# Performance work log

Measured on AMD Instinct MI355X. Metric: run time of the kernel, lower is better.

## Reference

```python
import jax, jax.numpy as jnp
import numpy as np

D_MODEL = 1024
NUM_HEADS = 16
D_K = D_MODEL // NUM_HEADS  # 64
B, T = 2, 2048


def rope_tables(seq_len, d_k):
    # Matches RotaryPositionalEmbedding + the slice apply_rotary takes:
    # only cos/sin of freqs (dim d_k//2) are used.
    half = d_k // 2
    inv_freq = 1.0 / (10000.0 ** (jnp.arange(0, d_k, 2, dtype=jnp.float32) / d_k))  # (half,)
    t = jnp.arange(seq_len, dtype=jnp.float32)
    freqs = jnp.einsum('i,j->ij', t, inv_freq)  # (T, half)
    return jnp.cos(freqs), jnp.sin(freqs)


def apply_rotary(x, cos, sin):
    # x: (B, H, T, D); rotate first 2*half dims as two halves
    half = x.shape[-1] // 2
    x1, x2 = x[..., :half], x[..., half:2 * half]
    c = cos[None, None, :x.shape[2], :half]
    s = sin[None, None, :x.shape[2], :half]
    return jnp.concatenate([x1 * c - x2 * s, x1 * s + x2 * c], axis=-1)


def setup_inputs() -> dict:
    key = jax.random.key(0)
    ks = jax.random.split(key, 5)
    scale = 1.0 / np.sqrt(D_MODEL)
    return {
        'x': jax.random.normal(ks[0], (B, T, D_MODEL), dtype=jnp.float32),
        'wq': jax.random.normal(ks[1], (D_MODEL, D_MODEL), dtype=jnp.float32) * scale,
        'wk': jax.random.normal(ks[2], (D_MODEL, D_MODEL), dtype=jnp.float32) * scale,
        'wv': jax.random.normal(ks[3], (D_MODEL, D_MODEL), dtype=jnp.float32) * scale,
        'wo': jax.random.normal(ks[4], (D_MODEL, D_MODEL), dtype=jnp.float32) * scale,
    }


def reference(x, wq, wk, wv, wo):
    Bs, Ts, _ = x.shape
    def proj(w):
        # nn.Linear: x @ w.T, then split heads -> (B, H, T, d_k)
        return (x @ w.T).reshape(Bs, Ts, NUM_HEADS, D_K).transpose(0, 2, 1, 3)
    Q, K, V = proj(wq), proj(wk), proj(wv)
    cos, sin = rope_tables(Ts, D_K)
    Q = apply_rotary(Q, cos, sin)
    K = apply_rotary(K, cos, sin)
    scores = jnp.einsum('bhqd,bhkd->bhqk', Q, K) / jnp.sqrt(jnp.float32(D_K))
    attn = jax.nn.softmax(scores, axis=-1)  # dropout is identity in eval
    out = jnp.einsum('bhqk,bhkd->bhqd', attn, V)
    out = out.transpose(0, 2, 1, 3).reshape(Bs, Ts, D_MODEL)
    return out @ wo.T
```

## Files before the change

### kernel.cpp

```cpp
#include <hip/hip_runtime.h>
#include <math.h>

typedef __attribute__((ext_vector_type(8))) short short8;
typedef __attribute__((ext_vector_type(4))) short short4v;
typedef __attribute__((ext_vector_type(4))) float f32x4;
typedef __attribute__((ext_vector_type(16))) float f32x16;

#define D_MODEL 1024
#define NUM_HEADS 16
#define D_K 64
#define B_SZ 2
#define T_SZ 2048
#define M_ROWS (B_SZ * T_SZ)
#define LSTR 72
#define LOG2E 1.4426950408889634f
#define KVSPLIT 1024

__device__ __forceinline__ unsigned short f2bf(float f) {
    union { float f; unsigned int u; } v; v.f = f;
    unsigned int r = v.u + 0x7FFF + ((v.u >> 16) & 1);
    return (unsigned short)(r >> 16);
}
__device__ __forceinline__ void gload_lds16(const void* g, void* l) {
    __builtin_amdgcn_global_load_lds(
        (const __attribute__((address_space(1))) unsigned int*)g,
        (__attribute__((address_space(3))) unsigned int*)l, 16, 0, 0);
}
__device__ __forceinline__ int cvtpk(float lo, float hi) {
    int r;
    asm("v_cvt_pk_bf16_f32 %0, %1, %2" : "=v"(r) : "v"(lo), "v"(hi));
    return r;
}

__global__ __launch_bounds__(256) void cvt_all(
    const float* __restrict__ x,  const float* __restrict__ w0,
    const float* __restrict__ w1, const float* __restrict__ w2,
    const float* __restrict__ w3, unsigned short* __restrict__ dst)
{
    const size_t NX8 = (size_t)M_ROWS * D_MODEL / 8;
    const size_t NW8 = (size_t)D_MODEL * D_MODEL / 8;
    size_t i = (size_t)blockIdx.x * 256 + threadIdx.x;
    const float* src; size_t off;
    if (i < NX8) { src = x; off = i; }
    else {
        size_t j = i - NX8;
        int ws = (int)(j >> 17);
        off = j & (NW8 - 1);
        src = (ws == 0) ? w0 : (ws == 1) ? w1 : (ws == 2) ? w2 : w3;
    }
    const float4* p = (const float4*)src + 2 * off;
    float4 a = p[0], b = p[1];
    short8 o;
    o[0] = f2bf(a.x); o[1] = f2bf(a.y); o[2] = f2bf(a.z); o[3] = f2bf(a.w);
    o[4] = f2bf(b.x); o[5] = f2bf(b.y); o[6] = f2bf(b.z); o[7] = f2bf(b.w);
    *((short8*)dst + i) = o;
}

__global__ __launch_bounds__(256) void rope_table(float2* __restrict__ tab)
{
    int idx = blockIdx.x * 256 + threadIdx.x;
    int t = idx >> 5, i = idx & 31;
    const float invf = (float)pow(10000.0, -(double)i / 32.0);
    float s, c;
    sincosf((float)t * invf, &s, &c);
    tab[idx] = make_float2(c, s);
}

__global__ __launch_bounds__(256) void gemm_qkv(
    const unsigned short* __restrict__ Xb,
    const unsigned short* __restrict__ Wq,
    const unsigned short* __restrict__ Wk,
    const unsigned short* __restrict__ Wv,
    unsigned short* __restrict__ Qb,
    unsigned short* __restrict__ Kb,
    unsigned short* __restrict__ Vtg,
    const float2* __restrict__ tab)
{
    const int z = blockIdx.z;
    const unsigned short* W = (z == 0) ? Wq : (z == 1) ? Wk : Wv;

    __shared__ unsigned short Als[2][128 * 32];
    __shared__ unsigned short Bls[2][128 * 32];

    const int tid = threadIdx.x;
    const int lane = tid & 63, wid = tid >> 6;
    const int g = lane >> 4, c16 = lane & 15;
    const int wr = wid >> 1, wc = wid & 1;
    const int m0 = blockIdx.y * 128, n0 = blockIdx.x * 128;

    const int sr = tid >> 2, sc = (tid & 3) * 8;
    const unsigned short* xg = Xb + (size_t)(m0 + sr) * D_MODEL + sc;
    const unsigned short* wg = W + (size_t)(n0 + sr) * D_MODEL + sc;

#define QKV_STAGE(bi, k0) do { \
    gload_lds16(xg + (k0), Als[bi] + wid * 512); \
    gload_lds16(xg + (k0) + (size_t)64 * D_MODEL, Als[bi] + wid * 512 + 2048); \
    gload_lds16(wg + (k0), Bls[bi] + wid * 512); \
    gload_lds16(wg + (k0) + (size_t)64 * D_MODEL, Bls[bi] + wid * 512 + 2048); \
  } while (0)

    f32x4 acc[4][4] = {};

    QKV_STAGE(0, 0);
    __syncthreads();
    for (int k0 = 0; k0 < D_MODEL; k0 += 32) {
        const int cur = (k0 >> 5) & 1;
        if (k0 + 32 < D_MODEL) QKV_STAGE(cur ^ 1, k0 + 32);
        short8 af[4], bf[4];
#pragma unroll
        for (int mf = 0; mf < 4; mf++)
            af[mf] = *(const short8*)&Als[cur][(wr * 64 + mf * 16 + c16) * 32 + g * 8];
#pragma unroll
        for (int nf = 0; nf < 4; nf++)
            bf[nf] = *(const short8*)&Bls[cur][(wc * 64 + nf * 16 + c16) * 32 + g * 8];
#pragma unroll
        for (int mf = 0; mf < 4; mf++)
#pragma unroll
            for (int nf = 0; nf < 4; nf++)
                acc[mf][nf] = __builtin_amdgcn_mfma_f32_16x16x32_bf16(
                    af[mf], bf[nf], acc[mf][nf], 0, 0, 0);
        __syncthreads();
    }

    if (z < 2) {
        const float qs = (z == 0) ? 0.125f * LOG2E : 1.0f;
        unsigned short* Y = (z == 0) ? Qb : Kb;
#pragma unroll
        for (int mf = 0; mf < 4; mf++)
#pragma unroll
            for (int j = 0; j < 4; j++) {
                int row = m0 + wr * 64 + mf * 16 + g * 4 + j;
                int t = row & (T_SZ - 1);
#pragma unroll
                for (int nf = 0; nf < 2; nf++) {
                    float2 cs = tab[t * 32 + nf * 16 + c16];
                    float a = acc[mf][nf][j], b2 = acc[mf][nf + 2][j];
                    acc[mf][nf][j]     = (a * cs.x - b2 * cs.y) * qs;
                    acc[mf][nf + 2][j] = (a * cs.y + b2 * cs.x) * qs;
                }
            }
#pragma unroll
        for (int mf = 0; mf < 4; mf++)
#pragma unroll
            for (int nf = 0; nf < 4; nf++)
#pragma unroll
                for (int j = 0; j < 4; j++) {
                    int row = m0 + wr * 64 + mf * 16 + g * 4 + j;
                    int col = n0 + wc * 64 + nf * 16 + c16;
                    Y[(size_t)row * D_MODEL + col] = f2bf(acc[mf][nf][j]);
                }
    } else {
#pragma unroll
        for (int mf = 0; mf < 4; mf++) {
            int row0 = m0 + wr * 64 + mf * 16 + g * 4;
            int bq = row0 >> 11;
            int t0 = row0 & (T_SZ - 1);
#pragma unroll
            for (int nf = 0; nf < 4; nf++) {
                int col = n0 + wc * 64 + nf * 16 + c16;
                int h = col >> 6, d = col & 63;
                short4v pk;
#pragma unroll
                for (int j = 0; j < 4; j++) pk[j] = (short)f2bf(acc[mf][nf][j]);
                *(short4v*)&Vtg[(size_t)((bq * 16 + h) * 64 + d) * T_SZ + t0] = pk;
            }
        }
    }
}

__global__ __launch_bounds__(256) void gemm_out(
    const unsigned short* __restrict__ Xb,
    const unsigned short* __restrict__ W,
    float* __restrict__ Y)
{
    __shared__ unsigned short Als[2][128 * 32];
    __shared__ unsigned short Bls[2][64 * 32];

    const int tid = threadIdx.x;
    const int lane = tid & 63, wid = tid >> 6;
    const int g = lane >> 4, c16 = lane & 15;
    const int wr = wid >> 1, wc = wid & 1;
    const int m0 = blockIdx.y * 128, n0 = blockIdx.x * 64;

    const int sr = tid >> 2, sc = (tid & 3) * 8;
    const unsigned short* xg = Xb + (size_t)(m0 + sr) * D_MODEL + sc;
    const unsigned short* wg = W + (size_t)(n0 + sr) * D_MODEL + sc;

#define OUT_STAGE(bi, k0) do { \
    gload_lds16(xg + (k0), Als[bi] + wid * 512); \
    gload_lds16(xg + (k0) + (size_t)64 * D_MODEL, Als[bi] + wid * 512 + 2048); \
    gload_lds16(wg + (k0), Bls[bi] + wid * 512); \
  } while (0)

    f32x4 acc[4][2] = {};

    OUT_STAGE(0, 0);
    __syncthreads();
    for (int k0 = 0; k0 < D_MODEL; k0 += 32) {
        const int cur = (k0 >> 5) & 1;
        if (k0 + 32 < D_MODEL) OUT_STAGE(cur ^ 1, k0 + 32);
        short8 af[4], bf[2];
#pragma unroll
        for (int mf = 0; mf < 4; mf++)
            af[mf] = *(const short8*)&Als[cur][(wr * 64 + mf * 16 + c16) * 32 + g * 8];
#pragma unroll
        for (int nf = 0; nf < 2; nf++)
            bf[nf] = *(const short8*)&Bls[cur][(wc * 32 + nf * 16 + c16) * 32 + g * 8];
#pragma unroll
        for (int mf = 0; mf < 4; mf++)
#pragma unroll
            for (int nf = 0; nf < 2; nf++)
                acc[mf][nf] = __builtin_amdgcn_mfma_f32_16x16x32_bf16(
                    af[mf], bf[nf], acc[mf][nf], 0, 0, 0);
        __syncthreads();
    }

#pragma unroll
    for (int mf = 0; mf < 4; mf++)
#pragma unroll
        for (int nf = 0; nf < 2; nf++)
#pragma unroll
            for (int j = 0; j < 4; j++) {
                int row = m0 + wr * 64 + mf * 16 + g * 4 + j;
                int col = n0 + wc * 32 + nf * 16 + c16;
                Y[(size_t)row * D_MODEL + col] = acc[mf][nf][j];
            }
}

#define PVAL(i) ((i) < 16 ? s0[(i) & 15] : s1[(i) & 15])

__global__ __launch_bounds__(512, 4) void attn_mfma32(
    const unsigned short* __restrict__ Qb,
    const unsigned short* __restrict__ Kb,
    const unsigned short* __restrict__ Vtg,
    unsigned short* __restrict__ Ob)
{
    __shared__ __align__(16) char smem[36864];

    const int tid = threadIdx.x;
    const int lane = tid & 63, wid = tid >> 6;
    const int kz = wid >> 2, wq = wid & 3;
    const int q32 = lane & 31, hi = lane >> 5;
    const int bh = blockIdx.y, b = bh >> 4, h = bh & (NUM_HEADS - 1);
    const int q0 = blockIdx.x * 128 + wq * 32;

    unsigned short* Ks = (unsigned short*)(smem + kz * 18432);
    unsigned short* Vt = Ks + 64 * LSTR;

    short8 qf[4];
    {
        const unsigned short* qsrc =
            Qb + (size_t)(b * T_SZ + q0 + q32) * D_MODEL + h * D_K + 8 * hi;
#pragma unroll
        for (int s = 0; s < 4; s++) qf[s] = *(const short8*)(qsrc + 16 * s);
    }

    f32x16 oacc0 = {}, oacc1 = {};
    float l = 0.f;

    const int t256 = tid & 255;
    const int krow = t256 >> 2, kcb = t256 & 3;
    const unsigned short* kbase =
        Kb + (size_t)(b * T_SZ + kz * KVSPLIT) * D_MODEL + h * D_K;
    const unsigned short* vtbase =
        Vtg + (size_t)((b * 16 + h) * 64) * T_SZ + kz * KVSPLIT;

    short8 pk0, pk1, pv0, pv1;
#define LOAD_KV(KT) do { \
    const unsigned short* _s = kbase + (size_t)((KT) + krow) * D_MODEL + kcb * 16; \
    pk0 = *(const short8*)_s; pk1 = *(const short8*)(_s + 8); \
    const unsigned short* _v = vtbase + (size_t)krow * T_SZ + (KT) + kcb * 16; \
    pv0 = *(const short8*)_v; pv1 = *(const short8*)(_v + 8); \
  } while (0)

    LOAD_KV(0);

    for (int kt = 0; kt < KVSPLIT; kt += 64) {
        __builtin_amdgcn_sched_barrier(0);
        __builtin_amdgcn_s_barrier();
        __builtin_amdgcn_sched_barrier(0);
        *(short8*)&Ks[krow * LSTR + kcb * 16] = pk0;
        *(short8*)&Ks[krow * LSTR + kcb * 16 + 8] = pk1;
        *(short8*)&Vt[krow * LSTR + kcb * 16] = pv0;
        *(short8*)&Vt[krow * LSTR + kcb * 16 + 8] = pv1;
        if (kt + 64 < KVSPLIT) LOAD_KV(kt + 64);
        asm volatile("s_waitcnt lgkmcnt(0)" ::: "memory");
        __builtin_amdgcn_s_barrier();
        __builtin_amdgcn_sched_barrier(0);

        f32x16 s0 = {}, s1 = {};
        __builtin_amdgcn_s_setprio(1);
#pragma unroll
        for (int s = 0; s < 4; s++) {
            short8 ak0 = *(const short8*)&Ks[q32 * LSTR + 16 * s + 8 * hi];
            short8 ak1 = *(const short8*)&Ks[(32 + q32) * LSTR + 16 * s + 8 * hi];
            s0 = __builtin_amdgcn_mfma_f32_32x32x16_bf16(ak0, qf[s], s0, 0, 0, 0);
            s1 = __builtin_amdgcn_mfma_f32_32x32x16_bf16(ak1, qf[s], s1, 0, 0, 0);
        }
        __builtin_amdgcn_s_setprio(0);

        float ps = 0.f;
#pragma unroll
        for (int r = 0; r < 16; r++) s0[r] = exp2f(s0[r]);
#pragma unroll
        for (int r = 0; r < 16; r++) s1[r] = exp2f(s1[r]);
#pragma unroll
        for (int r = 0; r < 16; r++) ps += s0[r] + s1[r];
        ps += __shfl_xor(ps, 32);
        l += ps;

        __builtin_amdgcn_s_setprio(1);
#pragma unroll
        for (int t = 0; t < 4; t++) {
            const int b0 = 4 * ((2 * t + 0) & 3) + 16 * (t >> 1);
            const int b1 = 4 * ((2 * t + 1) & 3) + 16 * (t >> 1);
            int X0 = cvtpk(PVAL(b0), PVAL(b0 + 1));
            int X1 = cvtpk(PVAL(b0 + 2), PVAL(b0 + 3));
            int Y0 = cvtpk(PVAL(b1), PVAL(b1 + 1));
            int Y1 = cvtpk(PVAL(b1 + 2), PVAL(b1 + 3));
            asm("v_permlane32_swap_b32 %0, %1" : "+v"(X0), "+v"(Y0));
            asm("v_permlane32_swap_b32 %0, %1" : "+v"(X1), "+v"(Y1));
            union { int w[4]; short8 v; } af;
            af.w[0] = X0; af.w[1] = X1; af.w[2] = Y0; af.w[3] = Y1;
            short8 bv0 = *(const short8*)&Vt[q32 * LSTR + 16 * t + 8 * hi];
            short8 bv1 = *(const short8*)&Vt[(32 + q32) * LSTR + 16 * t + 8 * hi];
            oacc0 = __builtin_amdgcn_mfma_f32_32x32x16_bf16(af.v, bv0, oacc0, 0, 0, 0);
            oacc1 = __builtin_amdgcn_mfma_f32_32x32x16_bf16(af.v, bv1, oacc1, 0, 0, 0);
        }
        __builtin_amdgcn_s_setprio(0);
    }

    __syncthreads();
    float* cmbO = (float*)smem;
    float* lb   = (float*)(smem + 32768);
    if (kz == 1) {
        if (hi == 0) lb[wq * 32 + q32] = l;
#pragma unroll
        for (int r = 0; r < 16; r++) {
            int qr = (r & 3) + 8 * (r >> 2) + 4 * hi;
            cmbO[wq * 2048 + qr * 64 + q32]      = oacc0[r];
            cmbO[wq * 2048 + qr * 64 + 32 + q32] = oacc1[r];
        }
    }
    __syncthreads();
    if (kz == 0) {
        float linv = 1.f / (l + lb[wq * 32 + q32]);
#pragma unroll
        for (int r = 0; r < 16; r++) {
            int qr = (r & 3) + 8 * (r >> 2) + 4 * hi;
            float iv = __shfl(linv, qr);
            float o0 = (oacc0[r] + cmbO[wq * 2048 + qr * 64 + q32]) * iv;
            float o1 = (oacc1[r] + cmbO[wq * 2048 + qr * 64 + 32 + q32]) * iv;
            size_t row = (size_t)(b * T_SZ + q0 + qr);
            Ob[row * D_MODEL + h * D_K + q32]      = f2bf(o0);
            Ob[row * D_MODEL + h * D_K + 32 + q32] = f2bf(o1);
        }
    }
}

extern "C" void kernel_launch(void* const* d_in, const int* in_sizes, int n_in,
                              void* d_out, int out_size, void* d_ws, size_t ws_size,
                              hipStream_t stream)
{
    const float* x  = (const float*)d_in[0];
    const float* wq = (const float*)d_in[1];
    const float* wk = (const float*)d_in[2];
    const float* wv = (const float*)d_in[3];
    const float* wo = (const float*)d_in[4];
    float* out = (float*)d_out;

    const size_t NX = (size_t)M_ROWS * D_MODEL;
    const size_t NW = (size_t)D_MODEL * D_MODEL;
    unsigned short* xb  = (unsigned short*)d_ws;
    unsigned short* wqb = xb + NX;
    unsigned short* wkb = wqb + NW;
    unsigned short* wvb = wkb + NW;
    unsigned short* wob = wvb + NW;
    unsigned short* Qb  = wob + NW;
    unsigned short* Kb  = Qb + NX;
    unsigned short* Vtg = Kb + NX;
    unsigned short* Ob  = Vtg + NX;
    float2* tab = (float2*)(Ob + NX);

    const int ncvt8 = (int)((NX + 4 * NW) / 8);
    cvt_all<<<dim3(ncvt8 / 256), dim3(256), 0, stream>>>(x, wq, wk, wv, wo, xb);
    rope_table<<<dim3(T_SZ * 32 / 256), dim3(256), 0, stream>>>(tab);

    gemm_qkv<<<dim3(D_MODEL / 128, M_ROWS / 128, 3), dim3(256), 0, stream>>>(
        xb, wqb, wkb, wvb, Qb, Kb, Vtg, tab);

    attn_mfma32<<<dim3(T_SZ / 128, B_SZ * NUM_HEADS), dim3(512), 0, stream>>>(
        Qb, Kb, Vtg, Ob);

    gemm_out<<<dim3(D_MODEL / 64, M_ROWS / 128), dim3(256), 0, stream>>>(Ob, wob, out);
}
```

Before: 223.0 us.

## Single-buffer GEMM LDS staging, use native exp2, hoist row-sum shuffle out of loop

Both projection GEMMs drop double-buffered LDS staging and instead load each K-slice into a single buffer between two barriers. This lowers LDS use, which may raise occupancy, but global loads no longer overlap the MFMA work. The attention kernel replaces exp2f with the hardware exp2 instruction, avoiding the denormal and range handling of the library call. It also moves the cross-half shuffle of the softmax row sum from every KV tile to once after the loop.

```diff
diff --git a/kernel.cpp b/kernel.cpp
--- a/kernel.cpp
+++ b/kernel.cpp
@@ -30,6 +30,13 @@
     int r;
     asm("v_cvt_pk_bf16_f32 %0, %1, %2" : "=v"(r) : "v"(lo), "v"(hi));
     return r;
+}
+__device__ __forceinline__ float fast_exp2(float x) {
+#if __has_builtin(__builtin_amdgcn_exp2f)
+    return __builtin_amdgcn_exp2f(x);
+#else
+    float r; asm("v_exp_f32 %0, %1" : "=v"(r) : "v"(x)); return r;
+#endif
 }
 
 __global__ __launch_bounds__(256) void cvt_all(
@@ -79,8 +86,8 @@
     const int z = blockIdx.z;
     const unsigned short* W = (z == 0) ? Wq : (z == 1) ? Wk : Wv;
 
-    __shared__ unsigned short Als[2][128 * 32];
-    __shared__ unsigned short Bls[2][128 * 32];
+    __shared__ unsigned short Als[128 * 32];
+    __shared__ unsigned short Bls[128 * 32];
 
     const int tid = threadIdx.x;
     const int lane = tid & 63, wid = tid >> 6;
@@ -91,35 +98,31 @@
     const int sr = tid >> 2, sc = (tid & 3) * 8;
     const unsigned short* xg = Xb + (size_t)(m0 + sr) * D_MODEL + sc;
     const unsigned short* wg = W + (size_t)(n0 + sr) * D_MODEL + sc;
-
-#define QKV_STAGE(bi, k0) do { \
-    gload_lds16(xg + (k0), Als[bi] + wid * 512); \
-    gload_lds16(xg + (k0) + (size_t)64 * D_MODEL, Als[bi] + wid * 512 + 2048); \
-    gload_lds16(wg + (k0), Bls[bi] + wid * 512); \
-    gload_lds16(wg + (k0) + (size_t)64 * D_MODEL, Bls[bi] + wid * 512 + 2048); \
-  } while (0)
+    unsigned short* adst = Als + wid * 512;
+    unsigned short* bdst = Bls + wid * 512;
 
     f32x4 acc[4][4] = {};
 
-    QKV_STAGE(0, 0);
-    __syncthreads();
     for (int k0 = 0; k0 < D_MODEL; k0 += 32) {
-        const int cur = (k0 >> 5) & 1;
-        if (k0 + 32 < D_MODEL) QKV_STAGE(cur ^ 1, k0 + 32);
+        __syncthreads();
+        gload_lds16(xg + k0, adst);
+        gload_lds16(xg + k0 + (size_t)64 * D_MODEL, adst + 2048);
+        gload_lds16(wg + k0, bdst);
+        gload_lds16(wg + k0 + (size_t)64 * D_MODEL, bdst + 2048);
+        __syncthreads();
         short8 af[4], bf[4];
 #pragma unroll
         for (int mf = 0; mf < 4; mf++)
-            af[mf] = *(const short8*)&Als[cur][(wr * 64 + mf * 16 + c16) * 32 + g * 8];
+            af[mf] = *(const short8*)&Als[(wr * 64 + mf * 16 + c16) * 32 + g * 8];
 #pragma unroll
         for (int nf = 0; nf < 4; nf++)
-            bf[nf] = *(const short8*)&Bls[cur][(wc * 64 + nf * 16 + c16) * 32 + g * 8];
+            bf[nf] = *(const short8*)&Bls[(wc * 64 + nf * 16 + c16) * 32 + g * 8];
 #pragma unroll
         for (int mf = 0; mf < 4; mf++)
 #pragma unroll
             for (int nf = 0; nf < 4; nf++)
                 acc[mf][nf] = __builtin_amdgcn_mfma_f32_16x16x32_bf16(
                     af[mf], bf[nf], acc[mf][nf], 0, 0, 0);
-        __syncthreads();
     }
 
     if (z < 2) {
@@ -173,8 +176,8 @@
     const unsigned short* __restrict__ W,
     float* __restrict__ Y)
 {
-    __shared__ unsigned short Als[2][128 * 32];
-    __shared__ unsigned short Bls[2][64 * 32];
+    __shared__ unsigned short Als[128 * 32];
+    __shared__ unsigned short Bls[64 * 32];
 
     const int tid = threadIdx.x;
     const int lane = tid & 63, wid = tid >> 6;
@@ -185,34 +188,30 @@
     const int sr = tid >> 2, sc = (tid & 3) * 8;
     const unsigned short* xg = Xb + (size_t)(m0 + sr) * D_MODEL + sc;
     const unsigned short* wg = W + (size_t)(n0 + sr) * D_MODEL + sc;
-
-#define OUT_STAGE(bi, k0) do { \
-    gload_lds16(xg + (k0), Als[bi] + wid * 512); \
-    gload_lds16(xg + (k0) + (size_t)64 * D_MODEL, Als[bi] + wid * 512 + 2048); \
-    gload_lds16(wg + (k0), Bls[bi] + wid * 512); \
-  } while (0)
+    unsigned short* adst = Als + wid * 512;
+    unsigned short* bdst = Bls + wid * 512;
 
     f32x4 acc[4][2] = {};
 
-    OUT_STAGE(0, 0);
-    __syncthreads();
     for (int k0 = 0; k0 < D_MODEL; k0 += 32) {
-        const int cur = (k0 >> 5) & 1;
-        if (k0 + 32 < D_MODEL) OUT_STAGE(cur ^ 1, k0 + 32);
+        __syncthreads();
+        gload_lds16(xg + k0, adst);
+        gload_lds16(xg + k0 + (size_t)64 * D_MODEL, adst + 2048);
+        gload_lds16(wg + k0, bdst);
+        __syncthreads();
         short8 af[4], bf[2];
 #pragma unroll
         for (int mf = 0; mf < 4; mf++)
-            af[mf] = *(const short8*)&Als[cur][(wr * 64 + mf * 16 + c16) * 32 + g * 8];
+            af[mf] = *(const short8*)&Als[(wr * 64 + mf * 16 + c16) * 32 + g * 8];
 #pragma unroll
         for (int nf = 0; nf < 2; nf++)
-            bf[nf] = *(const short8*)&Bls[cur][(wc * 32 + nf * 16 + c16) * 32 + g * 8];
+            bf[nf] = *(const short8*)&Bls[(wc * 32 + nf * 16 + c16) * 32 + g * 8];
 #pragma unroll
         for (int mf = 0; mf < 4; mf++)
 #pragma unroll
             for (int nf = 0; nf < 2; nf++)
                 acc[mf][nf] = __builtin_amdgcn_mfma_f32_16x16x32_bf16(
                     af[mf], bf[nf], acc[mf][nf], 0, 0, 0);
-        __syncthreads();
     }
 
 #pragma unroll
@@ -301,12 +300,11 @@
 
         float ps = 0.f;
 #pragma unroll
-        for (int r = 0; r < 16; r++) s0[r] = exp2f(s0[r]);
-#pragma unroll
-        for (int r = 0; r < 16; r++) s1[r] = exp2f(s1[r]);
+        for (int r = 0; r < 16; r++) s0[r] = fast_exp2(s0[r]);
+#pragma unroll
+        for (int r = 0; r < 16; r++) s1[r] = fast_exp2(s1[r]);
 #pragma unroll
         for (int r = 0; r < 16; r++) ps += s0[r] + s1[r];
-        ps += __shfl_xor(ps, 32);
         l += ps;
 
         __builtin_amdgcn_s_setprio(1);
@@ -330,6 +328,8 @@
         __builtin_amdgcn_s_setprio(0);
     }
 
+    l += __shfl_xor(l, 32);
+
     __syncthreads();
     float* cmbO = (float*)smem;
     float* lb   = (float*)(smem + 32768);
```

Measured after the change: 200.7 us. -10.0%, faster.
